# Performance work log

Measured on AMD Instinct MI355X. Metric: run time of the kernel, lower is better.

## Reference

```python
import jax, jax.numpy as jnp
import numpy as np

B, V, N, C = 32, 5, 196, 768
H = 768          # hidden_dim of score MLP
NUM_ITERS = 3


def setup_inputs() -> dict:
    key = jax.random.key(0)
    ks = jax.random.split(key, 6)
    scale = 1.0 / np.sqrt(C)
    x = jax.random.normal(ks[0], (B, V, N, C), dtype=jnp.float32)
    # per-view projection weights, stacked: [V, C, C] (no bias)
    w_views = jax.random.uniform(ks[1], (V, C, C), dtype=jnp.float32, minval=-scale, maxval=scale)
    # score MLP: Linear(2C -> H), Tanh, Linear(H -> 1)
    s1 = 1.0 / np.sqrt(2 * C)
    w1 = jax.random.uniform(ks[2], (2 * C, H), dtype=jnp.float32, minval=-s1, maxval=s1)
    b1 = jax.random.uniform(ks[3], (H,), dtype=jnp.float32, minval=-s1, maxval=s1)
    s2 = 1.0 / np.sqrt(H)
    w2 = jax.random.uniform(ks[4], (H, 1), dtype=jnp.float32, minval=-s2, maxval=s2)
    b2 = jax.random.uniform(ks[5], (1,), dtype=jnp.float32, minval=-s2, maxval=s2)
    return {"x": x, "w_views": w_views, "w1": w1, "b1": b1, "w2": w2, "b2": b2}


def reference(x, w_views, w1, b1, w2, b2):
    # x: [B, V, N, C]
    c = x.mean(axis=1)                                   # [B, N, C]
    # per-view projections are independent of c: compute once (same math)
    proj_x = jnp.einsum('bvnc,vcd->bvnd', x, w_views)    # [B, V, N, C]
    a = None
    for _ in range(NUM_ITERS):
        c_exp = jnp.broadcast_to(c[:, None], x.shape)    # [B, V, N, C]
        si = jnp.concatenate([x, c_exp], axis=-1)        # [B, V, N, 2C]
        h = jnp.tanh(jnp.einsum('bvnk,kh->bvnh', si, w1) + b1)
        s = (jnp.einsum('bvnh,ho->bvno', h, w2) + b2)[..., 0]  # [B, V, N]
        a = jax.nn.softmax(s, axis=1)                    # softmax over views
        c = jnp.einsum('bvn,bvnc->bnc', a, proj_x)       # weighted sum over V
    eps = 1e-8
    entropy = -(a * jnp.log(a + eps)).sum(axis=1)        # [B, N]
    r = 1.0 - entropy / np.log(V)
    return c, r
```

## Files before the change

kernel.cpp:

```cpp
#include <hip/hip_runtime.h>

#define CDIM   768
#define NSEQ   196
#define NVIEW  5
#define BN_TOT 6272
#define SLAB   4816896
#define WSLAB  589824

typedef __attribute__((ext_vector_type(8))) short short8;
typedef __attribute__((ext_vector_type(4))) float f32x4;

__device__ __forceinline__ float bf_lo(unsigned u) { return __uint_as_float(u << 16); }
__device__ __forceinline__ float bf_hi(unsigned u) { return __uint_as_float(u & 0xffff0000u); }
__device__ __forceinline__ unsigned short f2bf(float f) {
  unsigned u = __float_as_uint(f);
  return (unsigned short)((u + 0x7fffu + ((u >> 16) & 1u)) >> 16);
}
__device__ __forceinline__ unsigned pack2(float f0, float f1) {
  return (unsigned)f2bf(f0) | ((unsigned)f2bf(f1) << 16);
}
__device__ __forceinline__ float ftanh(float x) {
  x = fminf(fmaxf(x, -10.f), 10.f);
  float e = __expf(2.f * x);
  return (e - 1.f) / (e + 1.f);
}
__device__ __forceinline__ void async_cp16(const void* g, void* l) {
  __builtin_amdgcn_global_load_lds((const __attribute__((address_space(1))) unsigned*)g,
                                   (__attribute__((address_space(3))) unsigned*)l, 16, 0, 0);
}

__global__ __launch_bounds__(256) void k_tr(const float* __restrict__ wv,
                                            const float* __restrict__ w1,
                                            unsigned short* __restrict__ wvT,
                                            unsigned short* __restrict__ w1aT,
                                            unsigned short* __restrict__ w1bT,
                                            unsigned short* __restrict__ wvB) {
  __shared__ float tile[32][33];
  const int m = blockIdx.z;
  const float* src;
  unsigned short* dst;
  unsigned short* dstB = nullptr;
  if (m < NVIEW)      { src = wv + (size_t)m * WSLAB; dst = wvT + (size_t)m * WSLAB;
                        dstB = wvB + (size_t)m * WSLAB; }
  else if (m == NVIEW){ src = w1;                     dst = w1aT; }
  else                { src = w1 + WSLAB;             dst = w1bT; }
  const int tx = threadIdx.x, ty = threadIdx.y;
  const int x0 = blockIdx.x * 32, y0 = blockIdx.y * 32;
#pragma unroll
  for (int i = 0; i < 4; ++i) {
    float v = src[(size_t)(y0 + ty + i * 8) * CDIM + x0 + tx];
    tile[ty + i * 8][tx] = v;
    if (dstB) dstB[(size_t)(y0 + ty + i * 8) * CDIM + x0 + tx] = f2bf(v);
  }
  __syncthreads();
#pragma unroll
  for (int i = 0; i < 4; ++i)
    dst[(size_t)(x0 + ty + i * 8) * CDIM + y0 + tx] = f2bf(tile[tx][ty + i * 8]);
}

__global__ __launch_bounds__(192) void k_mean(const float* __restrict__ x,
                                              unsigned short* __restrict__ cb) {
  const int bn = blockIdx.x;
  const int b = bn / NSEQ, n = bn % NSEQ;
  const int h = threadIdx.x * 4;
  const float* xp = x + ((size_t)(b * NVIEW) * NSEQ + n) * CDIM + h;
  float s0 = 0, s1 = 0, s2 = 0, s3 = 0;
#pragma unroll
  for (int v = 0; v < NVIEW; ++v) {
    float4 p = *(const float4*)(xp + (size_t)v * (NSEQ * CDIM));
    s0 += p.x; s1 += p.y; s2 += p.z; s3 += p.w;
  }
  uint2 o;
  o.x = pack2(s0 * 0.2f, s1 * 0.2f);
  o.y = pack2(s2 * 0.2f, s3 * 0.2f);
  *(uint2*)(cb + (size_t)bn * CDIM + h) = o;
}

template <int MODE>
__global__ __launch_bounds__(512, 4) void gemm_f(const float* __restrict__ X,
                                                 const unsigned short* __restrict__ P0,
                                                 const unsigned short* __restrict__ P1,
                                                 const unsigned short* __restrict__ P2,
                                                 unsigned short* __restrict__ Q0,
                                                 unsigned short* __restrict__ Q1,
                                                 unsigned short* __restrict__ Q2) {
  __shared__ __align__(16) unsigned short lds[2 * 12288];
  constexpr int NWG = (MODE == 0) ? 2205 : (MODE == 1) ? 90 : 147;
  constexpr int NKT = CDIM / 32;
  const int orig = blockIdx.x;
  const int qq = NWG >> 3, rr = NWG & 7, xcd = orig & 7, slot = orig >> 3;
  const int wk = (xcd < rr ? xcd * (qq + 1) : rr * (qq + 1) + (xcd - rr) * qq) + slot;

  const int t = threadIdx.x, w = t >> 6, lane = t & 63, lr = lane & 15, lq = lane >> 4;
  const int wm = ((w >> 2) & 1) * 64;
  const int wn = (w & 3) * 64;

  const unsigned short* Abf = nullptr;
  const unsigned short* Bt;
  unsigned short* C;
  const float* aPtr = nullptr;
  int colBase, mrow0;
  if constexpr (MODE == 0) {
    const int v = wk / 441, rem = wk % 441;
    const int mt = rem / 9, nt = rem % 9;
    const int sub = nt / 3, ntl = nt % 3;
    Bt = (sub == 0) ? P0 + (size_t)v * WSLAB : (sub == 1) ? P1 : P2 + (size_t)v * WSLAB;
    C  = (sub == 0) ? Q0 + (size_t)v * SLAB  : (sub == 1) ? Q1 + (size_t)v * SLAB
                                             : Q2 + (size_t)v * SLAB;
    colBase = ntl * 256; mrow0 = mt * 128;
    const int r = mrow0 + (t >> 2);
    const int b = r / 196, n = r - b * 196;
    aPtr = X + (size_t)((b * 5 + v) * 196 + n) * CDIM + (t & 3) * 8;
  } else if constexpr (MODE == 1) {
    const int v = wk / 18, rem = wk % 18;
    const int mt = rem / 3, nt = rem % 3;
    Abf = P0;
    Bt  = P2 + (size_t)v * WSLAB;
    C   = Q0 + (size_t)v * WSLAB;
    colBase = nt * 256; mrow0 = mt * 128;
  } else {
    const int mt = wk / 3, nt = wk % 3;
    Abf = P1;
    Bt  = P0;
    C   = Q0;
    colBase = nt * 256; mrow0 = mt * 128;
  }

  const int swz = ((t & 3) ^ ((t >> 3) & 3)) << 3;
  const unsigned short* gBp = Bt + (size_t)(colBase + (t >> 2)) * CDIM + swz;
  const unsigned short* gAb = (MODE == 0) ? nullptr
                            : Abf + (size_t)(mrow0 + (t >> 2)) * CDIM + swz;
  const int aswz = swz;

  const int kch = ((lq ^ ((lr >> 1) & 3)) << 3);

#define STB(kt, s) { const unsigned short* sp_ = gBp + (kt) * 32;                 \
    unsigned short* dp_ = lds + (s) * 12288 + 4096 + (w << 9);                    \
    async_cp16(sp_, dp_); async_cp16(sp_ + (size_t)128 * CDIM, dp_ + 4096); }
#define STA1(kt, s) { async_cp16(gAb + (kt) * 32, lds + (s) * 12288 + (w << 9)); }
#define STA0W(s) { uint4 qv_;                                                     \
    qv_.x = pack2(pa0.x, pa0.y); qv_.y = pack2(pa0.z, pa0.w);                     \
    qv_.z = pack2(pa1.x, pa1.y); qv_.w = pack2(pa1.z, pa1.w);                     \
    *(uint4*)(lds + (s) * 12288 + (t >> 2) * 32 + aswz) = qv_; }

  f32x4 acc[4][4] = {};
  float4 pa0{}, pa1{};

  if constexpr (MODE == 0) { pa0 = *(const float4*)(aPtr); pa1 = *(const float4*)(aPtr + 4); }
  else                     { STA1(0, 0); }
  STB(0, 0);
  if constexpr (MODE == 0) STA0W(0);
  asm volatile("s_waitcnt vmcnt(0) lgkmcnt(0)" ::: "memory");
  __builtin_amdgcn_s_barrier();

  for (int kt = 0; kt < NKT; ++kt) {
    const int s = kt & 1;
    const unsigned short* bp = lds + s * 12288;
    const bool pf = (kt + 1 < NKT);
    if (pf) {
      if constexpr (MODE == 0) {
        pa0 = *(const float4*)(aPtr + (kt + 1) * 32);
        pa1 = *(const float4*)(aPtr + (kt + 1) * 32 + 4);
      } else { STA1(kt + 1, s ^ 1); }
      STB(kt + 1, s ^ 1);
    }
    short8 af[4], bf[4];
#pragma unroll
    for (int i = 0; i < 4; ++i) af[i] = *(const short8*)(bp + (wm + i * 16 + lr) * 32 + kch);
#pragma unroll
    for (int j = 0; j < 4; ++j) bf[j] = *(const short8*)(bp + 4096 + (wn + j * 16 + lr) * 32 + kch);
    __builtin_amdgcn_s_setprio(1);
#pragma unroll
    for (int i = 0; i < 4; ++i)
#pragma unroll
      for (int j = 0; j < 4; ++j)
        acc[i][j] = __builtin_amdgcn_mfma_f32_16x16x32_bf16(af[i], bf[j], acc[i][j], 0, 0, 0);
    __builtin_amdgcn_s_setprio(0);
    if (pf) { if constexpr (MODE == 0) STA0W(s ^ 1); }
    asm volatile("s_waitcnt vmcnt(0) lgkmcnt(0)" ::: "memory");
    __builtin_amdgcn_s_barrier();
  }
#undef STB
#undef STA1
#undef STA0W

#pragma unroll
  for (int i = 0; i < 4; ++i)
#pragma unroll
    for (int j = 0; j < 4; ++j) {
      const int gr = mrow0 + wm + i * 16 + lq * 4;
      const int gc = colBase + wn + j * 16 + lr;
      unsigned short* cp = C + (size_t)gr * CDIM + gc;
#pragma unroll
      for (int r = 0; r < 4; ++r)
        cp[(size_t)r * CDIM] = f2bf(acc[i][j][r]);
    }
}

__global__ __launch_bounds__(192) void k_iter3(const unsigned short* __restrict__ xw1b,
                                               const unsigned short* __restrict__ cw1,
                                               const unsigned short* __restrict__ pw1b,
                                               const unsigned short* __restrict__ projb,
                                               const float* __restrict__ b1,
                                               const float* __restrict__ w2,
                                               float* __restrict__ outc,
                                               float* __restrict__ outr) {
  __shared__ float red[3][NVIEW];
  __shared__ float aa[NVIEW];
  const int bn = blockIdx.x, t = threadIdx.x, wid = t >> 6, lane = t & 63;
  const int h = t * 4;
  const float4 bv = *(const float4*)(b1 + h);
  const float4 wv = *(const float4*)(w2 + h);
  float cw[4];
  { uint2 c = *(const uint2*)(cw1 + (size_t)bn * CDIM + h);
    cw[0] = bf_lo(c.x); cw[1] = bf_hi(c.x); cw[2] = bf_lo(c.y); cw[3] = bf_hi(c.y); }
  float xw[NVIEW][4], pf[NVIEW][4];
#pragma unroll
  for (int v = 0; v < NVIEW; ++v) {
    uint2 q = *(const uint2*)(xw1b + ((size_t)v * BN_TOT + bn) * CDIM + h);
    xw[v][0] = bf_lo(q.x) + bv.x; xw[v][1] = bf_hi(q.x) + bv.y;
    xw[v][2] = bf_lo(q.y) + bv.z; xw[v][3] = bf_hi(q.y) + bv.w;
    uint2 p = *(const uint2*)(pw1b + ((size_t)v * BN_TOT + bn) * CDIM + h);
    pf[v][0] = bf_lo(p.x); pf[v][1] = bf_hi(p.x);
    pf[v][2] = bf_lo(p.y); pf[v][3] = bf_hi(p.y);
  }
  for (int it = 0; it < 3; ++it) {
    float part[NVIEW];
#pragma unroll
    for (int v = 0; v < NVIEW; ++v) {
      float p;
      p = wv.x * ftanh(xw[v][0] + cw[0]);
      p = fmaf(wv.y, ftanh(xw[v][1] + cw[1]), p);
      p = fmaf(wv.z, ftanh(xw[v][2] + cw[2]), p);
      p = fmaf(wv.w, ftanh(xw[v][3] + cw[3]), p);
      part[v] = p;
    }
#pragma unroll
    for (int off = 32; off > 0; off >>= 1)
#pragma unroll
      for (int v = 0; v < NVIEW; ++v) part[v] += __shfl_down(part[v], off);
    if (lane == 0)
#pragma unroll
      for (int v = 0; v < NVIEW; ++v) red[wid][v] = part[v];
    __syncthreads();
    if (t == 0) {
      float s[NVIEW];
#pragma unroll
      for (int v = 0; v < NVIEW; ++v) s[v] = red[0][v] + red[1][v] + red[2][v];
      float m = s[0];
#pragma unroll
      for (int v = 1; v < NVIEW; ++v) m = fmaxf(m, s[v]);
      float a[NVIEW], sum = 0.f;
#pragma unroll
      for (int v = 0; v < NVIEW; ++v) { a[v] = __expf(s[v] - m); sum += a[v]; }
      const float inv = 1.f / sum;
#pragma unroll
      for (int v = 0; v < NVIEW; ++v) { a[v] *= inv; aa[v] = a[v]; }
      if (it == 2) {
        float ent = 0.f;
#pragma unroll
        for (int v = 0; v < NVIEW; ++v) ent -= a[v] * logf(a[v] + 1e-8f);
        outr[bn] = 1.f - ent * 0.6213349345596119f;
      }
    }
    __syncthreads();
    if (it < 2) {
      float n0 = 0, n1 = 0, n2 = 0, n3 = 0;
#pragma unroll
      for (int v = 0; v < NVIEW; ++v) {
        const float av = aa[v];
        n0 = fmaf(av, pf[v][0], n0); n1 = fmaf(av, pf[v][1], n1);
        n2 = fmaf(av, pf[v][2], n2); n3 = fmaf(av, pf[v][3], n3);
      }
      cw[0] = n0; cw[1] = n1; cw[2] = n2; cw[3] = n3;
    } else {
      float r0 = 0, r1 = 0, r2 = 0, r3 = 0;
#pragma unroll
      for (int v = 0; v < NVIEW; ++v) {
        const float av = aa[v];
        uint2 p = *(const uint2*)(projb + ((size_t)v * BN_TOT + bn) * CDIM + h);
        r0 = fmaf(av, bf_lo(p.x), r0); r1 = fmaf(av, bf_hi(p.x), r1);
        r2 = fmaf(av, bf_lo(p.y), r2); r3 = fmaf(av, bf_hi(p.y), r3);
      }
      float4 of; of.x = r0; of.y = r1; of.z = r2; of.w = r3;
      *(float4*)(outc + (size_t)bn * CDIM + h) = of;
    }
  }
}

extern "C" void kernel_launch(void* const* d_in, const int* in_sizes, int n_in,
                              void* d_out, int out_size, void* d_ws, size_t ws_size,
                              hipStream_t stream) {
  (void)in_sizes; (void)n_in; (void)out_size; (void)ws_size;
  const float* x  = (const float*)d_in[0];
  const float* wv = (const float*)d_in[1];
  const float* w1 = (const float*)d_in[2];
  const float* b1 = (const float*)d_in[3];
  const float* w2 = (const float*)d_in[4];

  unsigned short* ws   = (unsigned short*)d_ws;
  unsigned short* wvT  = ws;
  unsigned short* w1aT = ws + 2949120;
  unsigned short* w1bT = ws + 3538944;
  unsigned short* projb= ws + 4128768;
  unsigned short* xw1b = ws + 28213248;
  unsigned short* wvB  = ws + 28213248;
  unsigned short* pw1b = ws + 52297728;
  unsigned short* cb   = ws + 76382208;
  unsigned short* cw1  = ws + 81199104;
  unsigned short* wpT  = ws + 81199104;

  float* outc = (float*)d_out;
  float* outr = outc + SLAB;

  k_tr<<<dim3(24, 24, 7), dim3(32, 8), 0, stream>>>(wv, w1, wvT, w1aT, w1bT, wvB);
  k_mean<<<BN_TOT, 192, 0, stream>>>(x, cb);
  gemm_f<1><<<90, 512, 0, stream>>>(nullptr, w1bT, nullptr, wvB, wpT, nullptr, nullptr);
  gemm_f<0><<<2205, 512, 0, stream>>>(x, wvT, w1aT, wpT, projb, xw1b, pw1b);
  gemm_f<2><<<147, 512, 0, stream>>>(nullptr, w1bT, cb, nullptr, cw1, nullptr, nullptr);
  k_iter3<<<BN_TOT, 192, 0, stream>>>(xw1b, cw1, pw1b, projb, b1, w2, outc, outr);
}
```

Baseline: 401.4 us.

## Shrink GEMM tiles to 128x128, merge mean into transpose and prep GEMMs

The main fused GEMM now uses 256-thread blocks with 128x128 tiles (4410 blocks) in place of 512-thread 128x256 tiles. The goal is better occupancy and load balance across CUs, with a matching XCD remap. The mean kernel runs as an extra z-slice of the weight-transpose launch, and the two small precompute GEMMs (W1b·Wv and c·W1b) share one launch, cutting kernel launches from six to four. The wpT scratch now lives in the output buffer, which k_iter3 overwrites later. Smaller tiles cost more global traffic per FLOP.

```diff
diff --git a/kernel.cpp b/kernel.cpp
--- a/kernel.cpp
+++ b/kernel.cpp
@@ -29,14 +29,40 @@
                                    (__attribute__((address_space(3))) unsigned*)l, 16, 0, 0);
 }
 
-__global__ __launch_bounds__(256) void k_tr(const float* __restrict__ wv,
-                                            const float* __restrict__ w1,
-                                            unsigned short* __restrict__ wvT,
-                                            unsigned short* __restrict__ w1aT,
-                                            unsigned short* __restrict__ w1bT,
-                                            unsigned short* __restrict__ wvB) {
+__global__ __launch_bounds__(256) void k_tr2(const float* __restrict__ wv,
+                                             const float* __restrict__ w1,
+                                             const float* __restrict__ x,
+                                             unsigned short* __restrict__ wvT,
+                                             unsigned short* __restrict__ w1aT,
+                                             unsigned short* __restrict__ w1bT,
+                                             unsigned short* __restrict__ wvB,
+                                             unsigned short* __restrict__ cb) {
+  const int m = blockIdx.z;
+  const int tx = threadIdx.x, ty = threadIdx.y, t = ty * 32 + tx;
+  if (m == 7) {
+    const int bidx = blockIdx.y * 24 + blockIdx.x;
+    if (t < 192) {
+      const int col = t * 4;
+      for (int i = 0; i < 11; ++i) {
+        const int bn = bidx * 11 + i;
+        if (bn >= BN_TOT) break;
+        const int b = bn / NSEQ, n = bn - b * NSEQ;
+        const float* xp = x + ((size_t)(b * NVIEW) * NSEQ + n) * CDIM + col;
+        float s0 = 0, s1 = 0, s2 = 0, s3 = 0;
+#pragma unroll
+        for (int v = 0; v < NVIEW; ++v) {
+          float4 p = *(const float4*)(xp + (size_t)v * (NSEQ * CDIM));
+          s0 += p.x; s1 += p.y; s2 += p.z; s3 += p.w;
+        }
+        uint2 o;
+        o.x = pack2(s0 * 0.2f, s1 * 0.2f);
+        o.y = pack2(s2 * 0.2f, s3 * 0.2f);
+        *(uint2*)(cb + (size_t)bn * CDIM + col) = o;
+      }
+    }
+    return;
+  }
   __shared__ float tile[32][33];
-  const int m = blockIdx.z;
   const float* src;
   unsigned short* dst;
   unsigned short* dstB = nullptr;
@@ -44,7 +70,6 @@
                         dstB = wvB + (size_t)m * WSLAB; }
   else if (m == NVIEW){ src = w1;                     dst = w1aT; }
   else                { src = w1 + WSLAB;             dst = w1bT; }
-  const int tx = threadIdx.x, ty = threadIdx.y;
   const int x0 = blockIdx.x * 32, y0 = blockIdx.y * 32;
 #pragma unroll
   for (int i = 0; i < 4; ++i) {
@@ -58,112 +83,45 @@
     dst[(size_t)(x0 + ty + i * 8) * CDIM + y0 + tx] = f2bf(tile[tx][ty + i * 8]);
 }
 
-__global__ __launch_bounds__(192) void k_mean(const float* __restrict__ x,
-                                              unsigned short* __restrict__ cb) {
-  const int bn = blockIdx.x;
-  const int b = bn / NSEQ, n = bn % NSEQ;
-  const int h = threadIdx.x * 4;
-  const float* xp = x + ((size_t)(b * NVIEW) * NSEQ + n) * CDIM + h;
-  float s0 = 0, s1 = 0, s2 = 0, s3 = 0;
-#pragma unroll
-  for (int v = 0; v < NVIEW; ++v) {
-    float4 p = *(const float4*)(xp + (size_t)v * (NSEQ * CDIM));
-    s0 += p.x; s1 += p.y; s2 += p.z; s3 += p.w;
-  }
-  uint2 o;
-  o.x = pack2(s0 * 0.2f, s1 * 0.2f);
-  o.y = pack2(s2 * 0.2f, s3 * 0.2f);
-  *(uint2*)(cb + (size_t)bn * CDIM + h) = o;
-}
-
-template <int MODE>
-__global__ __launch_bounds__(512, 4) void gemm_f(const float* __restrict__ X,
-                                                 const unsigned short* __restrict__ P0,
-                                                 const unsigned short* __restrict__ P1,
-                                                 const unsigned short* __restrict__ P2,
-                                                 unsigned short* __restrict__ Q0,
-                                                 unsigned short* __restrict__ Q1,
-                                                 unsigned short* __restrict__ Q2) {
-  __shared__ __align__(16) unsigned short lds[2 * 12288];
-  constexpr int NWG = (MODE == 0) ? 2205 : (MODE == 1) ? 90 : 147;
-  constexpr int NKT = CDIM / 32;
-  const int orig = blockIdx.x;
-  const int qq = NWG >> 3, rr = NWG & 7, xcd = orig & 7, slot = orig >> 3;
-  const int wk = (xcd < rr ? xcd * (qq + 1) : rr * (qq + 1) + (xcd - rr) * qq) + slot;
-
+__global__ __launch_bounds__(256, 4) void k_pre(const unsigned short* __restrict__ w1bT,
+                                                const unsigned short* __restrict__ wvB,
+                                                const unsigned short* __restrict__ cb,
+                                                unsigned short* __restrict__ wpT,
+                                                unsigned short* __restrict__ cw1) {
+  __shared__ __align__(16) unsigned short lds[16384];
+  const int wk = blockIdx.x;
   const int t = threadIdx.x, w = t >> 6, lane = t & 63, lr = lane & 15, lq = lane >> 4;
-  const int wm = ((w >> 2) & 1) * 64;
-  const int wn = (w & 3) * 64;
-
-  const unsigned short* Abf = nullptr;
-  const unsigned short* Bt;
+  const int wm = (w >> 1) * 64, wn = (w & 1) * 64;
+  const unsigned short *Abf, *Bt;
   unsigned short* C;
-  const float* aPtr = nullptr;
-  int colBase, mrow0;
-  if constexpr (MODE == 0) {
-    const int v = wk / 441, rem = wk % 441;
-    const int mt = rem / 9, nt = rem % 9;
-    const int sub = nt / 3, ntl = nt % 3;
-    Bt = (sub == 0) ? P0 + (size_t)v * WSLAB : (sub == 1) ? P1 : P2 + (size_t)v * WSLAB;
-    C  = (sub == 0) ? Q0 + (size_t)v * SLAB  : (sub == 1) ? Q1 + (size_t)v * SLAB
-                                             : Q2 + (size_t)v * SLAB;
-    colBase = ntl * 256; mrow0 = mt * 128;
-    const int r = mrow0 + (t >> 2);
-    const int b = r / 196, n = r - b * 196;
-    aPtr = X + (size_t)((b * 5 + v) * 196 + n) * CDIM + (t & 3) * 8;
-  } else if constexpr (MODE == 1) {
-    const int v = wk / 18, rem = wk % 18;
-    const int mt = rem / 3, nt = rem % 3;
-    Abf = P0;
-    Bt  = P2 + (size_t)v * WSLAB;
-    C   = Q0 + (size_t)v * WSLAB;
-    colBase = nt * 256; mrow0 = mt * 128;
+  int mrow0, colBase;
+  if (wk < 180) {
+    const int v = wk / 36, rem = wk % 36;
+    mrow0 = (rem / 6) * 128; colBase = (rem % 6) * 128;
+    Abf = w1bT; Bt = wvB + (size_t)v * WSLAB; C = wpT + (size_t)v * WSLAB;
   } else {
-    const int mt = wk / 3, nt = wk % 3;
-    Abf = P1;
-    Bt  = P0;
-    C   = Q0;
-    colBase = nt * 256; mrow0 = mt * 128;
-  }
-
+    const int j = wk - 180;
+    mrow0 = (j / 6) * 128; colBase = (j % 6) * 128;
+    Abf = cb; Bt = w1bT; C = cw1;
+  }
   const int swz = ((t & 3) ^ ((t >> 3) & 3)) << 3;
-  const unsigned short* gBp = Bt + (size_t)(colBase + (t >> 2)) * CDIM + swz;
-  const unsigned short* gAb = (MODE == 0) ? nullptr
-                            : Abf + (size_t)(mrow0 + (t >> 2)) * CDIM + swz;
-  const int aswz = swz;
-
+  const unsigned short* gA = Abf + (size_t)(mrow0 + (t >> 2)) * CDIM + swz;
+  const unsigned short* gB = Bt + (size_t)(colBase + (t >> 2)) * CDIM + swz;
   const int kch = ((lq ^ ((lr >> 1) & 3)) << 3);
-
-#define STB(kt, s) { const unsigned short* sp_ = gBp + (kt) * 32;                 \
-    unsigned short* dp_ = lds + (s) * 12288 + 4096 + (w << 9);                    \
-    async_cp16(sp_, dp_); async_cp16(sp_ + (size_t)128 * CDIM, dp_ + 4096); }
-#define STA1(kt, s) { async_cp16(gAb + (kt) * 32, lds + (s) * 12288 + (w << 9)); }
-#define STA0W(s) { uint4 qv_;                                                     \
-    qv_.x = pack2(pa0.x, pa0.y); qv_.y = pack2(pa0.z, pa0.w);                     \
-    qv_.z = pack2(pa1.x, pa1.y); qv_.w = pack2(pa1.z, pa1.w);                     \
-    *(uint4*)(lds + (s) * 12288 + (t >> 2) * 32 + aswz) = qv_; }
-
+#define CPA(kt, s) { unsigned short* d_ = lds + (s) * 8192 + (w << 9);                  \
+    async_cp16(gA + (kt) * 32, d_);                                                     \
+    async_cp16(gA + (kt) * 32 + (size_t)64 * CDIM, d_ + 2048); }
+#define CPB(kt, s) { unsigned short* d_ = lds + (s) * 8192 + 4096 + (w << 9);           \
+    async_cp16(gB + (kt) * 32, d_);                                                     \
+    async_cp16(gB + (kt) * 32 + (size_t)64 * CDIM, d_ + 2048); }
   f32x4 acc[4][4] = {};
-  float4 pa0{}, pa1{};
-
-  if constexpr (MODE == 0) { pa0 = *(const float4*)(aPtr); pa1 = *(const float4*)(aPtr + 4); }
-  else                     { STA1(0, 0); }
-  STB(0, 0);
-  if constexpr (MODE == 0) STA0W(0);
-  asm volatile("s_waitcnt vmcnt(0) lgkmcnt(0)" ::: "memory");
+  CPA(0, 0); CPB(0, 0);
+  asm volatile("s_waitcnt vmcnt(0)" ::: "memory");
   __builtin_amdgcn_s_barrier();
-
-  for (int kt = 0; kt < NKT; ++kt) {
+  for (int kt = 0; kt < 24; ++kt) {
     const int s = kt & 1;
-    const unsigned short* bp = lds + s * 12288;
-    const bool pf = (kt + 1 < NKT);
-    if (pf) {
-      if constexpr (MODE == 0) {
-        pa0 = *(const float4*)(aPtr + (kt + 1) * 32);
-        pa1 = *(const float4*)(aPtr + (kt + 1) * 32 + 4);
-      } else { STA1(kt + 1, s ^ 1); }
-      STB(kt + 1, s ^ 1);
-    }
+    const unsigned short* bp = lds + s * 8192;
+    if (kt < 23) { CPA(kt + 1, s ^ 1); CPB(kt + 1, s ^ 1); }
     short8 af[4], bf[4];
 #pragma unroll
     for (int i = 0; i < 4; ++i) af[i] = *(const short8*)(bp + (wm + i * 16 + lr) * 32 + kch);
@@ -176,14 +134,11 @@
       for (int j = 0; j < 4; ++j)
         acc[i][j] = __builtin_amdgcn_mfma_f32_16x16x32_bf16(af[i], bf[j], acc[i][j], 0, 0, 0);
     __builtin_amdgcn_s_setprio(0);
-    if (pf) { if constexpr (MODE == 0) STA0W(s ^ 1); }
     asm volatile("s_waitcnt vmcnt(0) lgkmcnt(0)" ::: "memory");
     __builtin_amdgcn_s_barrier();
   }
-#undef STB
-#undef STA1
-#undef STA0W
-
+#undef CPA
+#undef CPB
 #pragma unroll
   for (int i = 0; i < 4; ++i)
 #pragma unroll
@@ -194,6 +149,89 @@
 #pragma unroll
       for (int r = 0; r < 4; ++r)
         cp[(size_t)r * CDIM] = f2bf(acc[i][j][r]);
+    }
+}
+
+__global__ __launch_bounds__(256, 4) void gemm_m(const float* __restrict__ X,
+                                                 const unsigned short* __restrict__ wvT,
+                                                 const unsigned short* __restrict__ w1aT,
+                                                 const unsigned short* __restrict__ wpT,
+                                                 unsigned short* __restrict__ projb,
+                                                 unsigned short* __restrict__ xw1b,
+                                                 unsigned short* __restrict__ pw1b) {
+  __shared__ __align__(16) unsigned short lds[16384];
+  const int orig = blockIdx.x;
+  const int xcd = orig & 7, slot0 = orig >> 3;
+  const int wk = (xcd < 2 ? xcd * 552 : 1104 + (xcd - 2) * 551) + slot0;
+  const int t = threadIdx.x, w = t >> 6, lane = t & 63, lr = lane & 15, lq = lane >> 4;
+  const int wm = (w >> 1) * 64, wn = (w & 1) * 64;
+  const int v = wk / 882, rem = wk % 882;
+  const int mt = rem / 18, qq = rem % 18, sub = qq / 6;
+  const int colBase = (qq % 6) * 128, mrow0 = mt * 128;
+  const unsigned short* Bt = sub == 0 ? wvT + (size_t)v * WSLAB
+                            : sub == 1 ? w1aT : wpT + (size_t)v * WSLAB;
+  unsigned short* C = (sub == 0 ? projb : sub == 1 ? xw1b : pw1b) + (size_t)v * SLAB;
+  const int r = mrow0 + (t >> 1), b = r / NSEQ, n = r - b * NSEQ;
+  const float* aRow = X + ((size_t)((b * NVIEW + v) * NSEQ) + n) * CDIM + (t & 1) * 16;
+  const int swz = ((t & 3) ^ ((t >> 3) & 3)) << 3;
+  const unsigned short* gB = Bt + (size_t)(colBase + (t >> 2)) * CDIM + swz;
+  const int sw = (t >> 2) & 3, c0 = (t & 1) * 2;
+  const int wA0 = (t >> 1) * 32 + ((c0 ^ sw) << 3);
+  const int wA1 = (t >> 1) * 32 + (((c0 + 1) ^ sw) << 3);
+  const int kch = ((lq ^ ((lr >> 1) & 3)) << 3);
+#define CPB(kt, s) { unsigned short* d_ = lds + (s) * 8192 + 4096 + (w << 9);           \
+    async_cp16(gB + (kt) * 32, d_);                                                     \
+    async_cp16(gB + (kt) * 32 + (size_t)64 * CDIM, d_ + 2048); }
+#define LOADA(kt) { f0 = *(const float4*)(aRow + (kt) * 32);                            \
+    f1 = *(const float4*)(aRow + (kt) * 32 + 4);                                        \
+    f2 = *(const float4*)(aRow + (kt) * 32 + 8);                                        \
+    f3 = *(const float4*)(aRow + (kt) * 32 + 12); }
+#define PACKW(s) { uint4 u0, u1;                                                        \
+    u0.x = pack2(f0.x, f0.y); u0.y = pack2(f0.z, f0.w);                                 \
+    u0.z = pack2(f1.x, f1.y); u0.w = pack2(f1.z, f1.w);                                 \
+    u1.x = pack2(f2.x, f2.y); u1.y = pack2(f2.z, f2.w);                                 \
+    u1.z = pack2(f3.x, f3.y); u1.w = pack2(f3.z, f3.w);                                 \
+    *(uint4*)(lds + (s) * 8192 + wA0) = u0;                                             \
+    *(uint4*)(lds + (s) * 8192 + wA1) = u1; }
+  f32x4 acc[4][4] = {};
+  float4 f0, f1, f2, f3;
+  LOADA(0); CPB(0, 0); PACKW(0);
+  asm volatile("s_waitcnt vmcnt(0) lgkmcnt(0)" ::: "memory");
+  __builtin_amdgcn_s_barrier();
+  for (int kt = 0; kt < 24; ++kt) {
+    const int s = kt & 1;
+    const unsigned short* bp = lds + s * 8192;
+    const bool pf = (kt < 23);
+    if (pf) { LOADA(kt + 1); CPB(kt + 1, s ^ 1); }
+    short8 af[4], bf[4];
+#pragma unroll
+    for (int i = 0; i < 4; ++i) af[i] = *(const short8*)(bp + (wm + i * 16 + lr) * 32 + kch);
+#pragma unroll
+    for (int j = 0; j < 4; ++j) bf[j] = *(const short8*)(bp + 4096 + (wn + j * 16 + lr) * 32 + kch);
+    __builtin_amdgcn_s_setprio(1);
+#pragma unroll
+    for (int i = 0; i < 4; ++i)
+#pragma unroll
+      for (int j = 0; j < 4; ++j)
+        acc[i][j] = __builtin_amdgcn_mfma_f32_16x16x32_bf16(af[i], bf[j], acc[i][j], 0, 0, 0);
+    __builtin_amdgcn_s_setprio(0);
+    if (pf) PACKW(s ^ 1);
+    asm volatile("s_waitcnt vmcnt(0) lgkmcnt(0)" ::: "memory");
+    __builtin_amdgcn_s_barrier();
+  }
+#undef CPB
+#undef LOADA
+#undef PACKW
+#pragma unroll
+  for (int i = 0; i < 4; ++i)
+#pragma unroll
+    for (int j = 0; j < 4; ++j) {
+      const int gr = mrow0 + wm + i * 16 + lq * 4;
+      const int gc = colBase + wn + j * 16 + lr;
+      unsigned short* cp = C + (size_t)gr * CDIM + gc;
+#pragma unroll
+      for (int rr = 0; rr < 4; ++rr)
+        cp[(size_t)rr * CDIM] = f2bf(acc[i][j][rr]);
     }
 }
 
@@ -308,15 +346,13 @@
   unsigned short* pw1b = ws + 52297728;
   unsigned short* cb   = ws + 76382208;
   unsigned short* cw1  = ws + 81199104;
-  unsigned short* wpT  = ws + 81199104;
 
   float* outc = (float*)d_out;
   float* outr = outc + SLAB;
-
-  k_tr<<<dim3(24, 24, 7), dim3(32, 8), 0, stream>>>(wv, w1, wvT, w1aT, w1bT, wvB);
-  k_mean<<<BN_TOT, 192, 0, stream>>>(x, cb);
-  gemm_f<1><<<90, 512, 0, stream>>>(nullptr, w1bT, nullptr, wvB, wpT, nullptr, nullptr);
-  gemm_f<0><<<2205, 512, 0, stream>>>(x, wvT, w1aT, wpT, projb, xw1b, pw1b);
-  gemm_f<2><<<147, 512, 0, stream>>>(nullptr, w1bT, cb, nullptr, cw1, nullptr, nullptr);
+  unsigned short* wpT  = (unsigned short*)d_out;
+
+  k_tr2<<<dim3(24, 24, 8), dim3(32, 8), 0, stream>>>(wv, w1, x, wvT, w1aT, w1bT, wvB, cb);
+  k_pre<<<474, 256, 0, stream>>>(w1bT, wvB, cb, wpT, cw1);
+  gemm_m<<<4410, 256, 0, stream>>>(x, wvT, w1aT, wpT, projb, xw1b, pw1b);
   k_iter3<<<BN_TOT, 192, 0, stream>>>(xw1b, cw1, pw1b, projb, b1, w2, outc, outr);
 }
```

New measurement: 436.3 us. 1.09x slower.
